# Performance work log

Measured on AMD Instinct MI355X. Metric: run time of the kernel, lower is better.

Reference implementation:

```python
import jax, jax.numpy as jnp
import numpy as np
import math

NUM_HEADS = 16
HEAD_SIZE = 64
BLOCK = 64          # SLA block size for pooled block scores / sparse selection
TOPK_RATIO = 0.1    # fraction of KV blocks attended per query block


def setup_inputs() -> dict:
    key = jax.random.key(0)
    kq, kk, kv = jax.random.split(key, 3)
    B, S, HD = 2, 4096, NUM_HEADS * HEAD_SIZE
    return {
        "query": jax.random.normal(kq, (B, S, HD), dtype=jnp.float32),
        "key": jax.random.normal(kk, (B, S, HD), dtype=jnp.float32),
        "value": jax.random.normal(kv, (B, S, HD), dtype=jnp.float32),
    }


def _sla_attention(q, k, v):
    # q, k, v: (B, H, S, D). Block-topk sparse attention (SLA-style):
    # mean-pool q/k per block, score blocks, keep top-k key blocks per
    # query block, gather only those K/V blocks, softmax over them.
    B, H, S, D = q.shape
    Nb = S // BLOCK
    scale = 1.0 / math.sqrt(D)

    qb = q.reshape(B, H, Nb, BLOCK, D)
    kb = k.reshape(B, H, Nb, BLOCK, D)
    vb = v.reshape(B, H, Nb, BLOCK, D)

    q_pool = qb.mean(axis=3)  # (B,H,Nb,D)
    k_pool = kb.mean(axis=3)  # (B,H,Nb,D)
    block_scores = jnp.einsum("bhid,bhjd->bhij", q_pool, k_pool) * scale

    K = max(1, int(math.ceil(TOPK_RATIO * Nb)))
    _, idx = jax.lax.top_k(block_scores, K)  # (B,H,Nb,K) selected key blocks

    # Gather selected key/value blocks: (B,H,Nb,K,BLOCK,D)
    gather_idx = idx[..., None, None]
    k_sel = jnp.take_along_axis(kb[:, :, None], gather_idx, axis=3)
    v_sel = jnp.take_along_axis(vb[:, :, None], gather_idx, axis=3)

    # Per-query-block scores over the K*BLOCK selected keys
    scores = jnp.einsum("bhnqd,bhnkjd->bhnqkj", qb, k_sel) * scale
    scores = scores.reshape(B, H, Nb, BLOCK, K * BLOCK)
    probs = jax.nn.softmax(scores, axis=-1)

    v_flat = v_sel.reshape(B, H, Nb, K * BLOCK, D)
    out = jnp.einsum("bhnqk,bhnkd->bhnqd", probs, v_flat)
    return out.reshape(B, H, S, D)


def reference(query, key, value):
    B, S, HD = query.shape
    H, D = NUM_HEADS, HEAD_SIZE
    # b s (h d) -> b h s d
    q = query.reshape(B, S, H, D).transpose(0, 2, 1, 3)
    k = key.reshape(B, S, H, D).transpose(0, 2, 1, 3)
    v = value.reshape(B, S, H, D).transpose(0, 2, 1, 3)
    out = _sla_attention(q, k, v)  # (B,H,S,D)
    # b h s d -> b s (h d)
    return out.transpose(0, 2, 1, 3).reshape(B, S, HD)
```

## Files before the change

### kernel.cpp

```cpp
#include <hip/hip_runtime.h>

constexpr int Bn = 2;
constexpr int Sn = 4096;
constexpr int Hh = 16;
constexpr int Dn = 64;
constexpr int HD = 1024;
constexpr int NB = 64;
constexpr int KS = 7;

typedef _Float16 f16x8 __attribute__((ext_vector_type(8)));
typedef _Float16 f16x4 __attribute__((ext_vector_type(4)));
typedef _Float16 f16x2 __attribute__((ext_vector_type(2)));
typedef __fp16   hf2   __attribute__((ext_vector_type(2)));
typedef float    f32x4 __attribute__((ext_vector_type(4)));

#define BARRIER_LDS() do { \
    asm volatile("s_waitcnt lgkmcnt(0)" ::: "memory"); \
    __builtin_amdgcn_s_barrier(); \
} while (0)

static __device__ __forceinline__ f16x8 cvt8(float4 a, float4 b) {
    f16x8 r;
    r[0] = (_Float16)a.x; r[1] = (_Float16)a.y;
    r[2] = (_Float16)a.z; r[3] = (_Float16)a.w;
    r[4] = (_Float16)b.x; r[5] = (_Float16)b.y;
    r[6] = (_Float16)b.z; r[7] = (_Float16)b.w;
    return r;
}

static __device__ __forceinline__ f16x4 pk4(float a, float b, float c, float d) {
    hf2 lo = __builtin_amdgcn_cvt_pkrtz(a, b);
    hf2 hi = __builtin_amdgcn_cvt_pkrtz(c, d);
    f16x2 l2 = __builtin_bit_cast(f16x2, lo);
    f16x2 h2 = __builtin_bit_cast(f16x2, hi);
    f16x4 r;
    r[0] = l2[0]; r[1] = l2[1]; r[2] = h2[0]; r[3] = h2[1];
    return r;
}

__global__ __launch_bounds__(64) void sla_pool(const float* __restrict__ Q,
                                               const float* __restrict__ K,
                                               float* __restrict__ qpool,
                                               float* __restrict__ kpool) {
    int bid  = blockIdx.x;
    int b    = bid / (Hh * NB);
    int rem  = bid % (Hh * NB);
    int h    = rem / NB;
    int nb   = rem % NB;
    int tid  = threadIdx.x;
    int quad = tid >> 4;
    int dq   = (tid & 15) << 2;

    const float* qb = Q + ((size_t)b * Sn + (size_t)nb * 64) * HD + h * Dn + dq;
    const float* kb = K + ((size_t)b * Sn + (size_t)nb * 64) * HD + h * Dn + dq;

    double sq[4] = {0, 0, 0, 0}, sk[4] = {0, 0, 0, 0};
    #pragma unroll
    for (int i = 0; i < 16; ++i) {
        size_t off = (size_t)(quad + i * 4) * HD;
        float4 x = *(const float4*)(qb + off);
        float4 y = *(const float4*)(kb + off);
        sq[0] += x.x; sq[1] += x.y; sq[2] += x.z; sq[3] += x.w;
        sk[0] += y.x; sk[1] += y.y; sk[2] += y.z; sk[3] += y.w;
    }
    #pragma unroll
    for (int j = 0; j < 4; ++j) {
        sq[j] += __shfl_xor(sq[j], 16); sq[j] += __shfl_xor(sq[j], 32);
        sk[j] += __shfl_xor(sk[j], 16); sk[j] += __shfl_xor(sk[j], 32);
    }
    if (quad == 0) {
        float4 oq, ok;
        oq.x = (float)(sq[0] * (1.0 / 64.0)); oq.y = (float)(sq[1] * (1.0 / 64.0));
        oq.z = (float)(sq[2] * (1.0 / 64.0)); oq.w = (float)(sq[3] * (1.0 / 64.0));
        ok.x = (float)(sk[0] * (1.0 / 64.0)); ok.y = (float)(sk[1] * (1.0 / 64.0));
        ok.z = (float)(sk[2] * (1.0 / 64.0)); ok.w = (float)(sk[3] * (1.0 / 64.0));
        *(float4*)(qpool + (size_t)bid * 64 + dq) = oq;
        *(float4*)(kpool + (size_t)bid * 64 + dq) = ok;
    }
}

__global__ __launch_bounds__(64) void sla_topk(const float* __restrict__ qpool,
                                               const float* __restrict__ kpool,
                                               int* __restrict__ topk) {
    int bid = blockIdx.x;
    int bh  = bid / NB;
    int j   = threadIdx.x;

    const float* qp = qpool + (size_t)bid * 64;
    const float* kp = kpool + ((size_t)bh * NB + j) * 64;
    double s = 0.0;
    #pragma unroll 8
    for (int d = 0; d < 64; ++d) s += (double)qp[d] * (double)kp[d];

    double v  = s;
    int   idx = j;
    #pragma unroll
    for (int it = 0; it < KS; ++it) {
        double bv = v; int bi = idx;
        #pragma unroll
        for (int off = 1; off < 64; off <<= 1) {
            double ov = __shfl_xor(bv, off);
            int    oi = __shfl_xor(bi, off);
            if (ov > bv || (ov == bv && oi < bi)) { bv = ov; bi = oi; }
        }
        if (j == 0) topk[(size_t)bid * KS + it] = bi;
        if (idx == bi) v = -1e300;
    }
}

__global__ __launch_bounds__(256) void sla_attn(const float* __restrict__ Q,
                                                const float* __restrict__ K,
                                                const float* __restrict__ V,
                                                const int* __restrict__ topk,
                                                float* __restrict__ O) {
    __shared__ _Float16 Ks[2][64][72];
    __shared__ _Float16 Vt[2][64][68];

    int raw = blockIdx.x;
    int bid = (raw & 7) * 256 + (raw >> 3);

    int b   = bid / (Hh * NB);
    int rem = bid % (Hh * NB);
    int h   = rem / NB;
    int nb  = rem % NB;

    int tid  = threadIdx.x;
    int w    = tid >> 6;
    int lane = tid & 63;
    int c    = lane & 15;
    int g    = lane >> 4;

    int skey = tid >> 2;
    int sd3  = tid & 3;
    int sdg  = sd3 << 4;
    int vcolB = skey ^ (sd3 << 4);
    int kch0 = ((sd3 << 1) + 0) ^ (skey & 7);
    int kch1 = ((sd3 << 1) + 1) ^ (skey & 7);
    int rch0 = (g + 0) ^ (c & 7);
    int rch1 = (g + 4) ^ (c & 7);
    int vrB  = (c & 3) << 2;

    int jidx[KS];
    {
        const int* tkp = topk + (size_t)bid * KS;
        #pragma unroll
        for (int i = 0; i < KS; ++i)
            jidx[i] = __builtin_amdgcn_readfirstlane(tkp[i]);
    }

    const float QS = 0.18033688f;
    f16x8 qf[2];
    {
        const float* qrow = Q + ((size_t)b * Sn + (size_t)nb * 64 + w * 16 + c) * HD + h * Dn;
        #pragma unroll
        for (int s2 = 0; s2 < 2; ++s2) {
            float4 a0 = *(const float4*)(qrow + s2 * 32 + g * 8);
            float4 a1 = *(const float4*)(qrow + s2 * 32 + g * 8 + 4);
            f16x8 q;
            q[0] = (_Float16)(a0.x * QS); q[1] = (_Float16)(a0.y * QS);
            q[2] = (_Float16)(a0.z * QS); q[3] = (_Float16)(a0.w * QS);
            q[4] = (_Float16)(a1.x * QS); q[5] = (_Float16)(a1.y * QS);
            q[6] = (_Float16)(a1.z * QS); q[7] = (_Float16)(a1.w * QS);
            qf[s2] = q;
        }
    }

    float rl = 0.f;
    f32x4 oacc[4];
    #pragma unroll
    for (int t = 0; t < 4; ++t) oacc[t] = f32x4{0.f, 0.f, 0.f, 0.f};

    const float* kbase = K + (size_t)b * Sn * HD + h * Dn;
    const float* vbase = V + (size_t)b * Sn * HD + h * Dn;

    float4 kx[4], vx[4];
    auto LOAD = [&](int blk) {
        const float* kp = kbase + ((size_t)blk * 64 + skey) * HD + sdg;
        const float* vp = vbase + ((size_t)blk * 64 + skey) * HD + sdg;
        #pragma unroll
        for (int i = 0; i < 4; ++i) kx[i] = *(const float4*)(kp + i * 4);
        #pragma unroll
        for (int i = 0; i < 4; ++i) vx[i] = *(const float4*)(vp + i * 4);
    };
    auto STAGE = [&](int buf) {
        *(f16x8*)&Ks[buf][skey][kch0 * 8] = cvt8(kx[0], kx[1]);
        *(f16x8*)&Ks[buf][skey][kch1 * 8] = cvt8(kx[2], kx[3]);
        #pragma unroll
        for (int i = 0; i < 4; ++i) {
            float4 v = vx[i];
            int db = sdg + i * 4;
            Vt[buf][db + 0][vcolB ^ 0 ] = (_Float16)v.x;
            Vt[buf][db + 1][vcolB ^ 4 ] = (_Float16)v.y;
            Vt[buf][db + 2][vcolB ^ 8 ] = (_Float16)v.z;
            Vt[buf][db + 3][vcolB ^ 12] = (_Float16)v.w;
        }
    };

    LOAD(jidx[0]);
    STAGE(0);
    LOAD(jidx[1]);
    BARRIER_LDS();

    #pragma unroll
    for (int kb = 0; kb < KS; ++kb) {
        const int cur = kb & 1;

        f32x4 sacc[4];
        #pragma unroll
        for (int t = 0; t < 4; ++t) sacc[t] = f32x4{0.f, 0.f, 0.f, 0.f};
        __builtin_amdgcn_s_setprio(1);
        #pragma unroll
        for (int t = 0; t < 4; ++t) {
            f16x8 a0 = *(const f16x8*)&Ks[cur][t * 16 + c][rch0 * 8];
            f16x8 a1 = *(const f16x8*)&Ks[cur][t * 16 + c][rch1 * 8];
            sacc[t] = __builtin_amdgcn_mfma_f32_16x16x32_f16(a0, qf[0], sacc[t], 0, 0, 0);
            sacc[t] = __builtin_amdgcn_mfma_f32_16x16x32_f16(a1, qf[1], sacc[t], 0, 0, 0);
        }
        __builtin_amdgcn_s_setprio(0);

        f16x4 e4[4];
        #pragma unroll
        for (int t = 0; t < 4; ++t) {
            float x0 = __builtin_amdgcn_exp2f(sacc[t][0]);
            float x1 = __builtin_amdgcn_exp2f(sacc[t][1]);
            float x2 = __builtin_amdgcn_exp2f(sacc[t][2]);
            float x3 = __builtin_amdgcn_exp2f(sacc[t][3]);
            rl += (x0 + x1) + (x2 + x3);
            e4[t] = pk4(x0, x1, x2, x3);
        }

        __builtin_amdgcn_s_setprio(1);
        #pragma unroll
        for (int t = 0; t < 4; ++t) {
            #pragma unroll
            for (int tt = 0; tt < 4; ++tt) {
                f16x4 va = *(const f16x4*)&Vt[cur][tt * 16 + c]
                               [((t * 16 + g * 4) ^ (tt << 4) ^ vrB)];
                oacc[tt] = __builtin_amdgcn_mfma_f32_16x16x16f16(va, e4[t], oacc[tt], 0, 0, 0);
            }
        }
        __builtin_amdgcn_s_setprio(0);

        if (kb + 1 < KS) {
            STAGE(cur ^ 1);
            if (kb + 2 < KS) LOAD(jidx[kb + 2]);
            BARRIER_LDS();
        }
    }

    rl += __shfl_xor(rl, 16);
    rl += __shfl_xor(rl, 32);

    float inv = 1.0f / rl;
    float* orow = O + ((size_t)b * Sn + (size_t)nb * 64 + w * 16 + c) * HD + h * Dn;
    #pragma unroll
    for (int t = 0; t < 4; ++t) {
        float4 o4;
        o4.x = oacc[t][0] * inv; o4.y = oacc[t][1] * inv;
        o4.z = oacc[t][2] * inv; o4.w = oacc[t][3] * inv;
        *(float4*)(orow + t * 16 + g * 4) = o4;
    }
}

extern "C" void kernel_launch(void* const* d_in, const int* in_sizes, int n_in,
                              void* d_out, int out_size, void* d_ws, size_t ws_size,
                              hipStream_t stream) {
    const float* Q = (const float*)d_in[0];
    const float* K = (const float*)d_in[1];
    const float* V = (const float*)d_in[2];
    float* O = (float*)d_out;

    float* qpool = (float*)d_ws;
    float* kpool = qpool + (size_t)Bn * Hh * NB * Dn;
    int*   topk  = (int*)(kpool + (size_t)Bn * Hh * NB * Dn);

    dim3 grid(Bn * Hh * NB);
    sla_pool<<<grid, 64, 0, stream>>>(Q, K, qpool, kpool);
    sla_topk<<<grid, 64, 0, stream>>>(qpool, kpool, topk);
    sla_attn<<<grid, 256, 0, stream>>>(Q, K, V, topk, O);
}
```

Baseline: 73.70 us.

## Use single-wave attention blocks with direct global-to-LDS fp32 K/V loads

Rewrites the attention kernel so that one 64-thread wave handles all 64 query rows of a block. K/V tiles are loaded as fp32 straight into LDS with global_load_lds, and the fp16 conversion happens when reading from LDS. This removes the register staging, the fp16 conversion pass on the way into LDS and the workgroup barriers. It also overlaps the next block's K/V loads with compute using vmcnt waits. In exchange, each wave holds four times the accumulators, fp32 LDS use doubles, and there are 4x fewer waves, which may reduce latency hiding.

```diff
diff --git a/kernel.cpp b/kernel.cpp
--- a/kernel.cpp
+++ b/kernel.cpp
@@ -13,11 +13,6 @@
 typedef _Float16 f16x2 __attribute__((ext_vector_type(2)));
 typedef __fp16   hf2   __attribute__((ext_vector_type(2)));
 typedef float    f32x4 __attribute__((ext_vector_type(4)));
-
-#define BARRIER_LDS() do { \
-    asm volatile("s_waitcnt lgkmcnt(0)" ::: "memory"); \
-    __builtin_amdgcn_s_barrier(); \
-} while (0)
 
 static __device__ __forceinline__ f16x8 cvt8(float4 a, float4 b) {
     f16x8 r;
@@ -108,13 +103,13 @@
     }
 }
 
-__global__ __launch_bounds__(256) void sla_attn(const float* __restrict__ Q,
-                                                const float* __restrict__ K,
-                                                const float* __restrict__ V,
-                                                const int* __restrict__ topk,
-                                                float* __restrict__ O) {
-    __shared__ _Float16 Ks[2][64][72];
-    __shared__ _Float16 Vt[2][64][68];
+__global__ __launch_bounds__(64) void sla_attn(const float* __restrict__ Q,
+                                               const float* __restrict__ K,
+                                               const float* __restrict__ V,
+                                               const int* __restrict__ topk,
+                                               float* __restrict__ O) {
+    __shared__ float Kl[4096];
+    __shared__ float Vl[4096];
 
     int raw = blockIdx.x;
     int bid = (raw & 7) * 256 + (raw >> 3);
@@ -124,142 +119,155 @@
     int h   = rem / NB;
     int nb  = rem % NB;
 
-    int tid  = threadIdx.x;
-    int w    = tid >> 6;
-    int lane = tid & 63;
+    int lane = threadIdx.x & 63;
     int c    = lane & 15;
     int g    = lane >> 4;
 
-    int skey = tid >> 2;
-    int sd3  = tid & 3;
-    int sdg  = sd3 << 4;
-    int vcolB = skey ^ (sd3 << 4);
-    int kch0 = ((sd3 << 1) + 0) ^ (skey & 7);
-    int kch1 = ((sd3 << 1) + 1) ^ (skey & 7);
-    int rch0 = (g + 0) ^ (c & 7);
-    int rch1 = (g + 4) ^ (c & 7);
-    int vrB  = (c & 3) << 2;
-
-    int jidx[KS];
-    {
-        const int* tkp = topk + (size_t)bid * KS;
-        #pragma unroll
-        for (int i = 0; i < KS; ++i)
-            jidx[i] = __builtin_amdgcn_readfirstlane(tkp[i]);
-    }
+    const int* tkp = topk + (size_t)bid * KS;
+    int j0 = __builtin_amdgcn_readfirstlane(tkp[0]);
+
+    const float* kbase = K + (size_t)b * Sn * HD + h * Dn;
+    const float* vbase = V + (size_t)b * Sn * HD + h * Dn;
+    const float* qbase = Q + ((size_t)b * Sn + (size_t)nb * 64) * HD + h * Dn;
+
+    int cx[4];
+    #pragma unroll
+    for (int j = 0; j < 4; ++j) cx[j] = (c ^ j) << 2;
+
+    #define ISSUE16(basep, blk, ldsarr) do {                                         \
+        const float* _bp = (basep) + ((size_t)(blk) * 64 + g) * HD;                  \
+        _Pragma("unroll")                                                            \
+        for (int _ch = 0; _ch < 16; ++_ch) {                                         \
+            const float* _src = _bp + (size_t)_ch * 4 * HD + cx[_ch & 3];            \
+            __builtin_amdgcn_global_load_lds(                                        \
+                (const __attribute__((address_space(1))) void*)_src,                 \
+                (__attribute__((address_space(3))) void*)&(ldsarr)[_ch * 256],       \
+                16, 0, 0);                                                           \
+        }                                                                            \
+    } while (0)
+
+    float4 qraw[4][2][2];
+    #pragma unroll
+    for (int f = 0; f < 4; ++f) {
+        const float* qrow = qbase + (size_t)(f * 16 + c) * HD;
+        #pragma unroll
+        for (int s2 = 0; s2 < 2; ++s2) {
+            qraw[f][s2][0] = *(const float4*)(qrow + s2 * 32 + g * 8);
+            qraw[f][s2][1] = *(const float4*)(qrow + s2 * 32 + g * 8 + 4);
+        }
+    }
+    ISSUE16(kbase, j0, Kl);
+    ISSUE16(vbase, j0, Vl);
 
     const float QS = 0.18033688f;
-    f16x8 qf[2];
-    {
-        const float* qrow = Q + ((size_t)b * Sn + (size_t)nb * 64 + w * 16 + c) * HD + h * Dn;
+    f16x8 qf[4][2];
+    #pragma unroll
+    for (int f = 0; f < 4; ++f) {
         #pragma unroll
         for (int s2 = 0; s2 < 2; ++s2) {
-            float4 a0 = *(const float4*)(qrow + s2 * 32 + g * 8);
-            float4 a1 = *(const float4*)(qrow + s2 * 32 + g * 8 + 4);
+            float4 a0 = qraw[f][s2][0], a1 = qraw[f][s2][1];
             f16x8 q;
             q[0] = (_Float16)(a0.x * QS); q[1] = (_Float16)(a0.y * QS);
             q[2] = (_Float16)(a0.z * QS); q[3] = (_Float16)(a0.w * QS);
             q[4] = (_Float16)(a1.x * QS); q[5] = (_Float16)(a1.y * QS);
             q[6] = (_Float16)(a1.z * QS); q[7] = (_Float16)(a1.w * QS);
-            qf[s2] = q;
-        }
-    }
-
-    float rl = 0.f;
-    f32x4 oacc[4];
-    #pragma unroll
-    for (int t = 0; t < 4; ++t) oacc[t] = f32x4{0.f, 0.f, 0.f, 0.f};
-
-    const float* kbase = K + (size_t)b * Sn * HD + h * Dn;
-    const float* vbase = V + (size_t)b * Sn * HD + h * Dn;
-
-    float4 kx[4], vx[4];
-    auto LOAD = [&](int blk) {
-        const float* kp = kbase + ((size_t)blk * 64 + skey) * HD + sdg;
-        const float* vp = vbase + ((size_t)blk * 64 + skey) * HD + sdg;
-        #pragma unroll
-        for (int i = 0; i < 4; ++i) kx[i] = *(const float4*)(kp + i * 4);
-        #pragma unroll
-        for (int i = 0; i < 4; ++i) vx[i] = *(const float4*)(vp + i * 4);
-    };
-    auto STAGE = [&](int buf) {
-        *(f16x8*)&Ks[buf][skey][kch0 * 8] = cvt8(kx[0], kx[1]);
-        *(f16x8*)&Ks[buf][skey][kch1 * 8] = cvt8(kx[2], kx[3]);
-        #pragma unroll
-        for (int i = 0; i < 4; ++i) {
-            float4 v = vx[i];
-            int db = sdg + i * 4;
-            Vt[buf][db + 0][vcolB ^ 0 ] = (_Float16)v.x;
-            Vt[buf][db + 1][vcolB ^ 4 ] = (_Float16)v.y;
-            Vt[buf][db + 2][vcolB ^ 8 ] = (_Float16)v.z;
-            Vt[buf][db + 3][vcolB ^ 12] = (_Float16)v.w;
-        }
-    };
-
-    LOAD(jidx[0]);
-    STAGE(0);
-    LOAD(jidx[1]);
-    BARRIER_LDS();
-
-    #pragma unroll
+            qf[f][s2] = q;
+        }
+    }
+
+    f32x4 oacc[4][4];
+    #pragma unroll
+    for (int f = 0; f < 4; ++f)
+        #pragma unroll
+        for (int tt = 0; tt < 4; ++tt) oacc[f][tt] = f32x4{0.f, 0.f, 0.f, 0.f};
+    float rl[4] = {0.f, 0.f, 0.f, 0.f};
+
+    int o1 = (g << 3) ^ ((c >> 2) << 2);
+    int vc = (g << 8) + (c ^ (g << 2));
+
     for (int kb = 0; kb < KS; ++kb) {
-        const int cur = kb & 1;
-
-        f32x4 sacc[4];
-        #pragma unroll
-        for (int t = 0; t < 4; ++t) sacc[t] = f32x4{0.f, 0.f, 0.f, 0.f};
-        __builtin_amdgcn_s_setprio(1);
+        int kn = (kb + 1 < KS) ? kb + 1 : 0;
+        int jn = __builtin_amdgcn_readfirstlane(tkp[kn]);
+
+        asm volatile("s_waitcnt vmcnt(16)" ::: "memory");
+
+        f32x4 sacc[4][4];
+        #pragma unroll
+        for (int f = 0; f < 4; ++f)
+            #pragma unroll
+            for (int t = 0; t < 4; ++t) sacc[f][t] = f32x4{0.f, 0.f, 0.f, 0.f};
         #pragma unroll
         for (int t = 0; t < 4; ++t) {
-            f16x8 a0 = *(const f16x8*)&Ks[cur][t * 16 + c][rch0 * 8];
-            f16x8 a1 = *(const f16x8*)&Ks[cur][t * 16 + c][rch1 * 8];
-            sacc[t] = __builtin_amdgcn_mfma_f32_16x16x32_f16(a0, qf[0], sacc[t], 0, 0, 0);
-            sacc[t] = __builtin_amdgcn_mfma_f32_16x16x32_f16(a1, qf[1], sacc[t], 0, 0, 0);
-        }
-        __builtin_amdgcn_s_setprio(0);
-
-        f16x4 e4[4];
-        #pragma unroll
-        for (int t = 0; t < 4; ++t) {
-            float x0 = __builtin_amdgcn_exp2f(sacc[t][0]);
-            float x1 = __builtin_amdgcn_exp2f(sacc[t][1]);
-            float x2 = __builtin_amdgcn_exp2f(sacc[t][2]);
-            float x3 = __builtin_amdgcn_exp2f(sacc[t][3]);
-            rl += (x0 + x1) + (x2 + x3);
-            e4[t] = pk4(x0, x1, x2, x3);
-        }
-
-        __builtin_amdgcn_s_setprio(1);
-        #pragma unroll
-        for (int t = 0; t < 4; ++t) {
-            #pragma unroll
-            for (int tt = 0; tt < 4; ++tt) {
-                f16x4 va = *(const f16x4*)&Vt[cur][tt * 16 + c]
-                               [((t * 16 + g * 4) ^ (tt << 4) ^ vrB)];
-                oacc[tt] = __builtin_amdgcn_mfma_f32_16x16x16f16(va, e4[t], oacc[tt], 0, 0, 0);
+            int rb = (t * 16 + c) * 64;
+            float4 ka0 = *(const float4*)&Kl[rb + o1];
+            float4 ka1 = *(const float4*)&Kl[rb + (o1 ^ 4)];
+            float4 kb0 = *(const float4*)&Kl[rb + 32 + o1];
+            float4 kb1 = *(const float4*)&Kl[rb + 32 + (o1 ^ 4)];
+            f16x8 a0 = cvt8(ka0, ka1);
+            f16x8 a1 = cvt8(kb0, kb1);
+            #pragma unroll
+            for (int f = 0; f < 4; ++f) {
+                sacc[f][t] = __builtin_amdgcn_mfma_f32_16x16x32_f16(a0, qf[f][0], sacc[f][t], 0, 0, 0);
+                sacc[f][t] = __builtin_amdgcn_mfma_f32_16x16x32_f16(a1, qf[f][1], sacc[f][t], 0, 0, 0);
             }
         }
-        __builtin_amdgcn_s_setprio(0);
-
-        if (kb + 1 < KS) {
-            STAGE(cur ^ 1);
-            if (kb + 2 < KS) LOAD(jidx[kb + 2]);
-            BARRIER_LDS();
-        }
-    }
-
-    rl += __shfl_xor(rl, 16);
-    rl += __shfl_xor(rl, 32);
-
-    float inv = 1.0f / rl;
-    float* orow = O + ((size_t)b * Sn + (size_t)nb * 64 + w * 16 + c) * HD + h * Dn;
-    #pragma unroll
-    for (int t = 0; t < 4; ++t) {
-        float4 o4;
-        o4.x = oacc[t][0] * inv; o4.y = oacc[t][1] * inv;
-        o4.z = oacc[t][2] * inv; o4.w = oacc[t][3] * inv;
-        *(float4*)(orow + t * 16 + g * 4) = o4;
-    }
+        asm volatile("s_waitcnt lgkmcnt(0)" ::: "memory");
+        if (kb + 1 < KS) ISSUE16(kbase, jn, Kl);
+
+        f16x4 e4[4][4];
+        #pragma unroll
+        for (int f = 0; f < 4; ++f) {
+            #pragma unroll
+            for (int t = 0; t < 4; ++t) {
+                float x0 = __builtin_amdgcn_exp2f(sacc[f][t][0]);
+                float x1 = __builtin_amdgcn_exp2f(sacc[f][t][1]);
+                float x2 = __builtin_amdgcn_exp2f(sacc[f][t][2]);
+                float x3 = __builtin_amdgcn_exp2f(sacc[f][t][3]);
+                rl[f] += (x0 + x1) + (x2 + x3);
+                e4[f][t] = pk4(x0, x1, x2, x3);
+            }
+        }
+
+        if (kb + 1 < KS) asm volatile("s_waitcnt vmcnt(16)" ::: "memory");
+        else             asm volatile("s_waitcnt vmcnt(0)"  ::: "memory");
+
+        #pragma unroll
+        for (int tt = 0; tt < 4; ++tt) {
+            #pragma unroll
+            for (int t = 0; t < 4; ++t) {
+                int base = t * 1024 + tt * 16 + vc;
+                float v0 = Vl[base];
+                float v1 = Vl[base + 64];
+                float v2 = Vl[base + 128];
+                float v3 = Vl[base + 192];
+                f16x4 va = pk4(v0, v1, v2, v3);
+                #pragma unroll
+                for (int f = 0; f < 4; ++f)
+                    oacc[f][tt] = __builtin_amdgcn_mfma_f32_16x16x16f16(va, e4[f][t], oacc[f][tt], 0, 0, 0);
+            }
+        }
+        asm volatile("s_waitcnt lgkmcnt(0)" ::: "memory");
+        if (kb + 1 < KS) ISSUE16(vbase, jn, Vl);
+    }
+
+    #pragma unroll
+    for (int f = 0; f < 4; ++f) {
+        rl[f] += __shfl_xor(rl[f], 16);
+        rl[f] += __shfl_xor(rl[f], 32);
+    }
+    #pragma unroll
+    for (int f = 0; f < 4; ++f) {
+        float inv = 1.0f / rl[f];
+        float* orow = O + ((size_t)b * Sn + (size_t)nb * 64 + f * 16 + c) * HD + h * Dn;
+        #pragma unroll
+        for (int tt = 0; tt < 4; ++tt) {
+            float4 o4;
+            o4.x = oacc[f][tt][0] * inv; o4.y = oacc[f][tt][1] * inv;
+            o4.z = oacc[f][tt][2] * inv; o4.w = oacc[f][tt][3] * inv;
+            *(float4*)(orow + tt * 16 + g * 4) = o4;
+        }
+    }
+    #undef ISSUE16
 }
 
 extern "C" void kernel_launch(void* const* d_in, const int* in_sizes, int n_in,
@@ -277,5 +285,5 @@
     dim3 grid(Bn * Hh * NB);
     sla_pool<<<grid, 64, 0, stream>>>(Q, K, qpool, kpool);
     sla_topk<<<grid, 64, 0, stream>>>(qpool, kpool, topk);
-    sla_attn<<<grid, 256, 0, stream>>>(Q, K, V, topk, O);
-}
+    sla_attn<<<grid, 64, 0, stream>>>(Q, K, V, topk, O);
+}
```

After: 74.24 us. No clear change (+0.7%).
